# Performance work log

Hardware: AMD Instinct MI355X
Metric: run time of the kernel (lower is better)

The kernel has to match this reference:

```python
import jax, jax.numpy as jnp
import numpy as np
from jax import lax

CLAMP = 4.135
OUT = 7            # RoI pool output size
SCALE = 1.0 / 16.0 # feature-map stride 16


def bilinear_gather(feat, bidx, y, x):
    """feat [B,C,H,W]; bidx [N] int; y,x [N,Ph,Pw] coords in feature space -> [N,C,Ph,Pw]."""
    B, C, H, W = feat.shape
    y = jnp.clip(y, 0.0, H - 1.0)
    x = jnp.clip(x, 0.0, W - 1.0)
    y0 = jnp.floor(y); x0 = jnp.floor(x)
    y0i = y0.astype(jnp.int32); x0i = x0.astype(jnp.int32)
    y1i = jnp.minimum(y0i + 1, H - 1); x1i = jnp.minimum(x0i + 1, W - 1)
    wy1 = y - y0; wx1 = x - x0
    wy0 = 1.0 - wy1; wx0 = 1.0 - wx1
    flat = feat.transpose(0, 2, 3, 1).reshape(B * H * W, C)
    base = (bidx * (H * W))[:, None, None]
    def g(yy, xx):
        return flat[base + yy * W + xx]  # [N,Ph,Pw,C]
    out = ((wy0 * wx0)[..., None] * g(y0i, x0i)
           + (wy0 * wx1)[..., None] * g(y0i, x1i)
           + (wy1 * wx0)[..., None] * g(y1i, x0i)
           + (wy1 * wx1)[..., None] * g(y1i, x1i))
    return out.transpose(0, 3, 1, 2)


def roi_align(feat, boxes, bidx):
    """RoIAlign, sampling_ratio=1 (one bilinear sample per bin center)."""
    N = boxes.shape[0]
    b = boxes * SCALE
    x1, y1, x2, y2 = b[:, 0], b[:, 1], b[:, 2], b[:, 3]
    bw = jnp.maximum(x2 - x1, 1.0) / OUT
    bh = jnp.maximum(y2 - y1, 1.0) / OUT
    c = jnp.arange(OUT, dtype=feat.dtype) + 0.5
    ys = y1[:, None] + c * bh[:, None]   # [N,OUT]
    xs = x1[:, None] + c * bw[:, None]
    yg = jnp.broadcast_to(ys[:, :, None], (N, OUT, OUT))
    xg = jnp.broadcast_to(xs[:, None, :], (N, OUT, OUT))
    return bilinear_gather(feat, bidx, yg, xg)


def xyxy_to_rbox(b):
    cx = (b[:, 0] + b[:, 2]) * 0.5
    cy = (b[:, 1] + b[:, 3]) * 0.5
    w = b[:, 2] - b[:, 0]
    h = b[:, 3] - b[:, 1]
    return jnp.stack([cx, cy, w, h, jnp.zeros_like(cx)], axis=1)


def decode_deltas_to_rboxes(rboxes, deltas):
    cx, cy, w, h, a = (rboxes[:, i] for i in range(5))
    dx, dy, dw, dh, da = (deltas[:, i] for i in range(5))
    return jnp.stack([cx + dx * w, cy + dy * h,
                      w * jnp.exp(dw), h * jnp.exp(dh), a + da], axis=1)


def grid_sample_zeros(feat, gx, gy):
    """F.grid_sample(bilinear, padding_mode='zeros', align_corners=False).
    feat [N,C,H,W]; gx,gy [N,Ho,Wo] normalized coords -> [N,C,Ho,Wo]."""
    N, C, H, W = feat.shape
    ix = ((gx + 1.0) * W - 1.0) * 0.5
    iy = ((gy + 1.0) * H - 1.0) * 0.5
    x0 = jnp.floor(ix); y0 = jnp.floor(iy)
    wx1 = ix - x0; wy1 = iy - y0
    x0i = x0.astype(jnp.int32); y0i = y0.astype(jnp.int32)
    flat = feat.transpose(0, 2, 3, 1).reshape(N, H * W, C)
    Ho, Wo = gx.shape[1], gx.shape[2]
    def g(yy, xx, wt):
        valid = ((yy >= 0) & (yy < H) & (xx >= 0) & (xx < W)).astype(feat.dtype)
        idx = jnp.clip(yy, 0, H - 1) * W + jnp.clip(xx, 0, W - 1)
        v = jnp.take_along_axis(flat, idx.reshape(N, -1, 1), axis=1)
        v = v.reshape(N, Ho, Wo, C)
        return (wt * valid)[..., None] * v
    out = (g(y0i, x0i, (1 - wy1) * (1 - wx1))
           + g(y0i, x0i + 1, (1 - wy1) * wx1)
           + g(y0i + 1, x0i, wy1 * (1 - wx1))
           + g(y0i + 1, x0i + 1, wy1 * wx1))
    return out.transpose(0, 3, 1, 2)


def setup_inputs() -> dict:
    key = jax.random.key(0)
    ks = jax.random.split(key, 12)
    B, C, H, W = 2, 256, 64, 64
    N, NC = 2048, 16
    FD = C * OUT * OUT  # 12544
    features = jax.random.normal(ks[0], (B, C, H, W), jnp.float32)
    # valid image-space boxes (image 1024x1024, stride-16 features)
    cx = jax.random.uniform(ks[1], (N,), minval=96.0, maxval=928.0)
    cy = jax.random.uniform(ks[2], (N,), minval=96.0, maxval=928.0)
    bw = jax.random.uniform(ks[3], (N,), minval=16.0, maxval=128.0)
    bh = jax.random.uniform(ks[4], (N,), minval=16.0, maxval=128.0)
    proposals = jnp.stack([cx - bw / 2, cy - bh / 2, cx + bw / 2, cy + bh / 2], axis=1)
    batch_idx = jnp.repeat(jnp.arange(B, dtype=jnp.int32), N // B)
    s = 0.02
    return {
        "features": features,
        "proposals": proposals,
        "batch_idx": batch_idx,
        "conv_w": jax.random.normal(ks[5], (C, C, 3, 3), jnp.float32) * s,
        "conv_b": jnp.zeros((C,), jnp.float32),
        "align_w": jax.random.normal(ks[6], (5, FD), jnp.float32) * s,
        "align_b": jnp.zeros((5,), jnp.float32),
        "fc1_w": jax.random.normal(ks[7], (1024, FD), jnp.float32) * s,
        "fc1_b": jnp.zeros((1024,), jnp.float32),
        "fc2_w": jax.random.normal(ks[8], (1024, 1024), jnp.float32) * s,
        "fc2_b": jnp.zeros((1024,), jnp.float32),
        "cls_w": jax.random.normal(ks[9], (NC, 1024), jnp.float32) * s,
        "cls_b": jnp.zeros((NC,), jnp.float32),
        "box_w": jax.random.normal(ks[10], (5, 1024), jnp.float32) * s,
        "box_b": jnp.zeros((5,), jnp.float32),
    }


def reference(features, proposals, batch_idx, conv_w, conv_b, align_w, align_b,
              fc1_w, fc1_b, fc2_w, fc2_b, cls_w, cls_b, box_w, box_b):
    N = proposals.shape[0]
    # 1) RoI align
    box_feat = roi_align(features, proposals, batch_idx)           # [N,256,7,7]
    a = lax.conv_general_dilated(box_feat, conv_w, (1, 1), ((1, 1), (1, 1)),
                                 dimension_numbers=("NCHW", "OIHW", "NCHW"))
    a = jax.nn.relu(a + conv_b[None, :, None, None]).reshape(N, -1)
    coarse = jnp.clip(a @ align_w.T + align_b, -CLAMP, CLAMP)      # [N,5]
    # 3) decode to rboxes (torch.no_grad -> stop_gradient)
    prop_rb = xyxy_to_rbox(proposals)
    align_rb = lax.stop_gradient(decode_deltas_to_rboxes(prop_rb, coarse))
    # 4) affine grid from rbox (no translation, matches source) + grid_sample
    w, h, ang = align_rb[:, 2], align_rb[:, 3], align_rb[:, 4]
    cth, sth = jnp.cos(ang), jnp.sin(ang)
    sx, sy = w / OUT, h / OUT
    base = (2.0 * jnp.arange(OUT, dtype=box_feat.dtype) + 1.0) / OUT - 1.0
    xb = base[None, None, :]
    yb = base[None, :, None]
    gx = (sx * cth)[:, None, None] * xb + (-(sy * sth))[:, None, None] * yb
    gy = (sx * sth)[:, None, None] * xb + (sy * cth)[:, None, None] * yb
    aligned = grid_sample_zeros(box_feat, gx, gy)                  # [N,256,7,7]
    # 5) refine head MLP + predictors
    r = jax.nn.relu(aligned.reshape(N, -1) @ fc1_w.T + fc1_b)
    r = jax.nn.relu(r @ fc2_w.T + fc2_b)
    logits = r @ cls_w.T + cls_b                                   # [N,16]
    final = jnp.clip(r @ box_w.T + box_b, -CLAMP, CLAMP)           # [N,5]
    # 6) eval-path decode + softmax (per-class NMS is dynamic-shape postproc, excluded)
    pred_rboxes = decode_deltas_to_rboxes(prop_rb, final)
    scores = jax.nn.softmax(logits, axis=-1)
    return jnp.concatenate([pred_rboxes, scores], axis=1)          # [N,21]
```

## Files before the change

kernel.cpp:

```cpp
#include <hip/hip_runtime.h>
#include <hip/hip_bf16.h>
#include <math.h>
#include <type_traits>

constexpr int B = 2, C = 256, H = 64, W = 64, HW = H * W;
constexpr int N = 2048, OUT = 7, P = 49, FD = C * P;
constexpr int K1 = 1024;
constexpr float CLAMP_V = 4.135f, SCALE_V = 1.0f / 16.0f;
constexpr int LDB = 264;

typedef short s8v __attribute__((ext_vector_type(8)));
typedef short s4v __attribute__((ext_vector_type(4)));
typedef float f32x4 __attribute__((ext_vector_type(4)));

template <int I, int NN, class F>
__device__ __forceinline__ void static_for(F&& f) {
    if constexpr (I < NN) {
        f(std::integral_constant<int, I>{});
        static_for<I + 1, NN>(static_cast<F&&>(f));
    }
}

__device__ __forceinline__ int xcd_swz(int blk, int nblk) {
    const int cpx = nblk >> 3;
    return (blk & 7) * cpx + (blk >> 3);
}

__global__ void k_prep_all(const float* __restrict__ features, float* __restrict__ featT,
                           const float* __restrict__ conv_w, __hip_bfloat16* __restrict__ wB,
                           const float* __restrict__ align_w, float4* __restrict__ aw4,
                           float* __restrict__ aw1,
                           const float* __restrict__ fc1_w, __hip_bfloat16* __restrict__ fc1B,
                           const float* __restrict__ fc2_w, __hip_bfloat16* __restrict__ fc2B) {
    __shared__ float smem[64 * 49];
    const int id = blockIdx.x;
    const int t = threadIdx.x;
    if (id < 2048) {
        const int x = id % 128, y = (id / 128) % 8, b = id / 1024;
        const int c0 = y * 32, p0 = x * 32;
        const int tx = t % 32, ty = t / 32;
        float* tile = smem;
#pragma unroll
        for (int r = 0; r < 32; r += 8)
            tile[(ty + r) * 33 + tx] = features[(size_t)(b * C + c0 + ty + r) * HW + p0 + tx];
        __syncthreads();
#pragma unroll
        for (int r = 0; r < 32; r += 8)
            featT[(size_t)(b * HW + p0 + ty + r) * C + c0 + tx] = tile[tx * 33 + ty + r];
    } else if (id < 2120) {
        const int T = id - 2048;
        const int tap = T / 8, s = T % 8;
        const int co = t;
#pragma unroll
        for (int q = 0; q < 4; ++q)
#pragma unroll
            for (int j = 0; j < 8; ++j) {
                const int ci = s * 32 + q * 8 + j;
                wB[(((size_t)T * 256 + co) * 4 + q) * 8 + j] =
                    __float2bfloat16(conv_w[(size_t)co * 2304 + ci * 9 + tap]);
            }
    } else if (id < 2169) {
        const int o = id - 2120;
        const int co = t;
        float4 v;
        v.x = align_w[(size_t)0 * FD + co * 49 + o];
        v.y = align_w[(size_t)1 * FD + co * 49 + o];
        v.z = align_w[(size_t)2 * FD + co * 49 + o];
        v.w = align_w[(size_t)3 * FD + co * 49 + o];
        aw4[o * 256 + co] = v;
        aw1[o * 256 + co] = align_w[(size_t)4 * FD + co * 49 + o];
    } else if (id < 6265) {
        const int q = id - 2169;
        const int c0 = (q % 4) * 64;
        const int o = q / 4;
        const float* src = fc1_w + (size_t)o * FD + (size_t)c0 * 49;
        for (int i = t; i < 64 * 49; i += 256) smem[i] = src[i];
        __syncthreads();
        __hip_bfloat16* dst = fc1B + (size_t)o * FD + c0;
        for (int j = t; j < 64 * 49; j += 256) {
            const int p = j >> 6, cc = j & 63;
            dst[(size_t)p * 256 + cc] = __float2bfloat16(smem[cc * 49 + p]);
        }
    } else {
        const int bid = id - 6265;
        const int n4 = (K1 * K1) / 4;
        for (int i = bid * 256 + t; i < n4; i += 256 * 256) {
            const float4 v = reinterpret_cast<const float4*>(fc2_w)[i];
            fc2B[i * 4 + 0] = __float2bfloat16(v.x);
            fc2B[i * 4 + 1] = __float2bfloat16(v.y);
            fc2B[i * 4 + 2] = __float2bfloat16(v.z);
            fc2B[i * 4 + 3] = __float2bfloat16(v.w);
        }
    }
}

__global__ __launch_bounds__(256, 2) void k_roi_conv_grid(
    const float* __restrict__ featT, const float* __restrict__ proposals,
    const int* __restrict__ bidx, const __hip_bfloat16* __restrict__ wB,
    const float* __restrict__ conv_b, const float4* __restrict__ aw4,
    const float* __restrict__ aw1, const float* __restrict__ align_b,
    __hip_bfloat16* __restrict__ alignedOut) {
    __shared__ __align__(16) __hip_bfloat16 bfh[100 * LDB];
    __shared__ float red[64];

    const int blk = xcd_swz(blockIdx.x, 1024);
    const int t = threadIdx.x;
    const int lane = t & 63, wid = t >> 6;
    const int l15 = lane & 15;
    const int qofs = (lane >> 4) * 8;

#pragma unroll
    for (int r = 0; r < 2; ++r) {
        const int n = blk * 2 + r;
        const float px1 = proposals[n * 4 + 0] * SCALE_V, py1 = proposals[n * 4 + 1] * SCALE_V;
        const float px2 = proposals[n * 4 + 2] * SCALE_V, py2 = proposals[n * 4 + 3] * SCALE_V;
        const float bw = fmaxf(px2 - px1, 1.0f) * (1.0f / OUT);
        const float bh = fmaxf(py2 - py1, 1.0f) * (1.0f / OUT);
        const int b = bidx[n];
        const float* fb = featT + (size_t)b * HW * C;
#pragma unroll 2
        for (int p = wid; p < P; p += 4) {
            const int pyi = p / 7, pxi = p % 7;
            float y = py1 + (pyi + 0.5f) * bh;
            float x = px1 + (pxi + 0.5f) * bw;
            y = fminf(fmaxf(y, 0.f), (float)(H - 1));
            x = fminf(fmaxf(x, 0.f), (float)(W - 1));
            const float y0f = floorf(y), x0f = floorf(x);
            const int y0 = (int)y0f, x0 = (int)x0f;
            const int y1 = min(y0 + 1, H - 1), x1 = min(x0 + 1, W - 1);
            const float wy1 = y - y0f, wx1 = x - x0f;
            const float wy0 = 1.f - wy1, wx0 = 1.f - wx1;
            const int c4 = lane * 4;
            const float4 v00 = *reinterpret_cast<const float4*>(&fb[(size_t)(y0 * W + x0) * C + c4]);
            const float4 v01 = *reinterpret_cast<const float4*>(&fb[(size_t)(y0 * W + x1) * C + c4]);
            const float4 v10 = *reinterpret_cast<const float4*>(&fb[(size_t)(y1 * W + x0) * C + c4]);
            const float4 v11 = *reinterpret_cast<const float4*>(&fb[(size_t)(y1 * W + x1) * C + c4]);
            s4v o4;
            o4[0] = (short)__bfloat16_as_ushort(__float2bfloat16(
                        wy0 * (wx0 * v00.x + wx1 * v01.x) + wy1 * (wx0 * v10.x + wx1 * v11.x)));
            o4[1] = (short)__bfloat16_as_ushort(__float2bfloat16(
                        wy0 * (wx0 * v00.y + wx1 * v01.y) + wy1 * (wx0 * v10.y + wx1 * v11.y)));
            o4[2] = (short)__bfloat16_as_ushort(__float2bfloat16(
                        wy0 * (wx0 * v00.z + wx1 * v01.z) + wy1 * (wx0 * v10.z + wx1 * v11.z)));
            o4[3] = (short)__bfloat16_as_ushort(__float2bfloat16(
                        wy0 * (wx0 * v00.w + wx1 * v01.w) + wy1 * (wx0 * v10.w + wx1 * v11.w)));
            *reinterpret_cast<s4v*>(&bfh[(2 * p + r) * LDB + c4]) = o4;
        }
    }
    bfh[98 * LDB + t] = __float2bfloat16(0.f);
    bfh[99 * LDB + t] = __float2bfloat16(0.f);
    __syncthreads();

    const int rp = l15 & 1;
    int oyt[7], oxt[7];
    bool pval[7];
    static_for<0, 7>([&](auto MT) {
        const int p = (MT.value * 16 + l15) >> 1;
        pval[MT.value] = (p < 49);
        oyt[MT.value] = p / 7;
        oxt[MT.value] = p % 7;
    });
    int bofs[4];
    static_for<0, 4>([&](auto NT) {
        const int col = wid * 64 + NT.value * 16 + l15;
        bofs[NT.value] = col * 32 + qofs;
    });

    f32x4 acc[7][4] = {};
    for (int tap = 0; tap < 9; ++tap) {
        const int dy = tap / 3 - 1, dx = tap % 3 - 1;
        int rsel[7];
        static_for<0, 7>([&](auto MT) {
            const int iy = oyt[MT.value] + dy, ix = oxt[MT.value] + dx;
            const bool v = pval[MT.value] && ((unsigned)iy < 7u) && ((unsigned)ix < 7u);
            rsel[MT.value] = (v ? (2 * (iy * 7 + ix) + rp) : (98 + rp)) * LDB;
        });
        const __hip_bfloat16* wTap = wB + (size_t)tap * 8 * 8192;
#pragma unroll
        for (int s = 0; s < 8; ++s) {
            s8v af[7], bfr[4];
            static_for<0, 4>([&](auto NT) {
                bfr[NT.value] = *reinterpret_cast<const s8v*>(&wTap[(size_t)s * 8192 + bofs[NT.value]]);
            });
            static_for<0, 7>([&](auto MT) {
                af[MT.value] = *reinterpret_cast<const s8v*>(&bfh[rsel[MT.value] + s * 32 + qofs]);
            });
            __builtin_amdgcn_s_setprio(1);
            static_for<0, 7>([&](auto MT) {
                static_for<0, 4>([&](auto NT) {
                    acc[MT.value][NT.value] = __builtin_amdgcn_mfma_f32_16x16x32_bf16(
                        af[MT.value], bfr[NT.value], acc[MT.value][NT.value], 0, 0, 0);
                });
            });
            __builtin_amdgcn_s_setprio(0);
        }
    }

    const int hi = lane >> 4;
    float cb[4];
    static_for<0, 4>([&](auto NT) { cb[NT.value] = conv_b[wid * 64 + NT.value * 16 + l15]; });
    float pc[2][5] = {};
    static_for<0, 7>([&](auto MT) {
        static_for<0, 4>([&](auto RR) {
            constexpr int r = RR.value & 1;
            const int p = MT.value * 8 + hi * 2 + (RR.value >> 1);
            if (p < 49) {
                static_for<0, 4>([&](auto NT) {
                    const int co = wid * 64 + NT.value * 16 + l15;
                    const float4 w4 = aw4[p * 256 + co];
                    const float  w1 = aw1[p * 256 + co];
                    const float a = fmaxf(acc[MT.value][NT.value][RR.value] + cb[NT.value], 0.f);
                    pc[r][0] = fmaf(a, w4.x, pc[r][0]);
                    pc[r][1] = fmaf(a, w4.y, pc[r][1]);
                    pc[r][2] = fmaf(a, w4.z, pc[r][2]);
                    pc[r][3] = fmaf(a, w4.w, pc[r][3]);
                    pc[r][4] = fmaf(a, w1,   pc[r][4]);
                });
            }
        });
    });
    static_for<0, 2>([&](auto RI) {
        static_for<0, 5>([&](auto J) {
            float s = pc[RI.value][J.value];
#pragma unroll
            for (int off = 32; off; off >>= 1) s += __shfl_xor(s, off);
            pc[RI.value][J.value] = s;
        });
        if (lane == 0) {
            static_for<0, 5>([&](auto J) { red[RI.value * 20 + wid * 5 + J.value] = pc[RI.value][J.value]; });
        }
    });
    __syncthreads();

    if (t < 2) {
        const int r = t;
        const int n = blk * 2 + r;
        float coarse[5];
        static_for<0, 5>([&](auto Jc) {
            constexpr int j = Jc.value;
            float s = red[r * 20 + j] + red[r * 20 + 5 + j] + red[r * 20 + 10 + j] +
                      red[r * 20 + 15 + j] + align_b[j];
            coarse[j] = fminf(fmaxf(s, -CLAMP_V), CLAMP_V);
        });
        const float x1r = proposals[n * 4 + 0], y1r = proposals[n * 4 + 1];
        const float x2r = proposals[n * 4 + 2], y2r = proposals[n * 4 + 3];
        const float w = x2r - x1r, h = y2r - y1r;
        const float w2 = w * expf(coarse[2]);
        const float h2 = h * expf(coarse[3]);
        const float ang = coarse[4];
        const float cth = cosf(ang), sth = sinf(ang);
        const float sx = w2 * (1.0f / OUT), sy = h2 * (1.0f / OUT);
        red[48 + r * 4 + 0] = sx * cth;
        red[48 + r * 4 + 1] = sy * sth;
        red[48 + r * 4 + 2] = sx * sth;
        red[48 + r * 4 + 3] = sy * cth;
    }
    __syncthreads();

#pragma unroll
    for (int r = 0; r < 2; ++r) {
        const float gA = red[48 + r * 4 + 0], gBv = red[48 + r * 4 + 1];
        const float gC = red[48 + r * 4 + 2], gD = red[48 + r * 4 + 3];
        __hip_bfloat16* ao = alignedOut + (size_t)(blk * 2 + r) * FD;
        const int c4 = lane * 4;
#pragma unroll 2
        for (int p = wid; p < P; p += 4) {
            const int pyi = p / 7, pxi = p % 7;
            const float xb = (2 * pxi + 1) * (1.0f / OUT) - 1.0f;
            const float yb = (2 * pyi + 1) * (1.0f / OUT) - 1.0f;
            const float gx = gA * xb - gBv * yb;
            const float gy = gC * xb + gD * yb;
            const float ix = ((gx + 1.0f) * OUT - 1.0f) * 0.5f;
            const float iy = ((gy + 1.0f) * OUT - 1.0f) * 0.5f;
            const float x0f = floorf(ix), y0f = floorf(iy);
            const int x0 = (int)x0f, y0 = (int)y0f;
            const float wx1 = ix - x0f, wy1 = iy - y0f;
            const float wx0 = 1.f - wx1, wy0 = 1.f - wy1;
            const float w00 = wy0 * wx0, w01 = wy0 * wx1, w10 = wy1 * wx0, w11 = wy1 * wx1;
            const bool vx0 = (unsigned)x0 < 7u, vx1 = (unsigned)(x0 + 1) < 7u;
            const bool vy0 = (unsigned)y0 < 7u, vy1 = (unsigned)(y0 + 1) < 7u;
            const int r00 = (vy0 && vx0) ? (y0 * 7 + x0) : 49;
            const int r01 = (vy0 && vx1) ? (y0 * 7 + x0 + 1) : 49;
            const int r10 = (vy1 && vx0) ? ((y0 + 1) * 7 + x0) : 49;
            const int r11 = (vy1 && vx1) ? ((y0 + 1) * 7 + x0 + 1) : 49;
            const s4v b00 = *reinterpret_cast<const s4v*>(&bfh[(2 * r00 + r) * LDB + c4]);
            const s4v b01 = *reinterpret_cast<const s4v*>(&bfh[(2 * r01 + r) * LDB + c4]);
            const s4v b10 = *reinterpret_cast<const s4v*>(&bfh[(2 * r10 + r) * LDB + c4]);
            const s4v b11 = *reinterpret_cast<const s4v*>(&bfh[(2 * r11 + r) * LDB + c4]);
            s4v o4;
            static_for<0, 4>([&](auto J) {
                constexpr int j = J.value;
                float v = w00 * __bfloat162float(__ushort_as_bfloat16((unsigned short)b00[j]))
                        + w01 * __bfloat162float(__ushort_as_bfloat16((unsigned short)b01[j]))
                        + w10 * __bfloat162float(__ushort_as_bfloat16((unsigned short)b10[j]))
                        + w11 * __bfloat162float(__ushort_as_bfloat16((unsigned short)b11[j]));
                o4[j] = (short)__bfloat16_as_ushort(__float2bfloat16(v));
            });
            *reinterpret_cast<s4v*>(&ao[p * 256 + c4]) = o4;
        }
    }
}

template <int BM, int BN, int BK>
__global__ __launch_bounds__(256, 4) void k_gemm_bf16(
    const __hip_bfloat16* __restrict__ A, const __hip_bfloat16* __restrict__ Wt,
    const float* __restrict__ bias, float* __restrict__ CoutF,
    __hip_bfloat16* __restrict__ CoutH, int M, int Nn, int K, int relu) {
    constexpr int LD = BK + 8;
    __shared__ __align__(16) __hip_bfloat16 As[2][BM * LD];
    __shared__ __align__(16) __hip_bfloat16 Ws[2][BN * LD];
    const int ntb = Nn / BN;
    const int blkS = xcd_swz(blockIdx.x, gridDim.x);
    const int bx = blkS % ntb, by = blkS / ntb;
    const int t = threadIdx.x;
    const int lane = t & 63, wid = t >> 6;
    const int l15 = lane & 15;
    const int qofs = (lane >> 4) * 8;
    const int wm = wid >> 1, wn = wid & 1;

    const int ar = t >> 3, ak = (t & 7) * 8;
    const size_t aBase = (size_t)(by * BM) * K;
    const size_t bBase = (size_t)(bx * BN) * K;

    f32x4 acc[2][2] = {};

    const int steps = K / BK;
    {
        const s8v a0 = *reinterpret_cast<const s8v*>(&A[aBase + (size_t)ar * K + ak]);
        const s8v a1 = *reinterpret_cast<const s8v*>(&A[aBase + (size_t)(ar + 32) * K + ak]);
        const s8v b0 = *reinterpret_cast<const s8v*>(&Wt[bBase + (size_t)ar * K + ak]);
        const s8v b1 = *reinterpret_cast<const s8v*>(&Wt[bBase + (size_t)(ar + 32) * K + ak]);
        *reinterpret_cast<s8v*>(&As[0][ar * LD + ak]) = a0;
        *reinterpret_cast<s8v*>(&As[0][(ar + 32) * LD + ak]) = a1;
        *reinterpret_cast<s8v*>(&Ws[0][ar * LD + ak]) = b0;
        *reinterpret_cast<s8v*>(&Ws[0][(ar + 32) * LD + ak]) = b1;
    }
    __syncthreads();

    for (int s = 0; s < steps; ++s) {
        const int cur = s & 1;
        const bool pf = (s + 1 < steps);
        s8v a0, a1, b0, b1;
        if (pf) {
            const int k0 = (s + 1) * BK;
            a0 = *reinterpret_cast<const s8v*>(&A[aBase + (size_t)ar * K + k0 + ak]);
            a1 = *reinterpret_cast<const s8v*>(&A[aBase + (size_t)(ar + 32) * K + k0 + ak]);
            b0 = *reinterpret_cast<const s8v*>(&Wt[bBase + (size_t)ar * K + k0 + ak]);
            b1 = *reinterpret_cast<const s8v*>(&Wt[bBase + (size_t)(ar + 32) * K + k0 + ak]);
        }
        static_for<0, 2>([&](auto KH) {
            s8v afr[2], bfr[2];
            static_for<0, 2>([&](auto MT) {
                afr[MT.value] = *reinterpret_cast<const s8v*>(
                    &As[cur][(wm * 32 + MT.value * 16 + l15) * LD + KH.value * 32 + qofs]);
            });
            static_for<0, 2>([&](auto NT) {
                bfr[NT.value] = *reinterpret_cast<const s8v*>(
                    &Ws[cur][(wn * 32 + NT.value * 16 + l15) * LD + KH.value * 32 + qofs]);
            });
            static_for<0, 2>([&](auto MT) {
                static_for<0, 2>([&](auto NT) {
                    acc[MT.value][NT.value] = __builtin_amdgcn_mfma_f32_16x16x32_bf16(
                        afr[MT.value], bfr[NT.value], acc[MT.value][NT.value], 0, 0, 0);
                });
            });
        });
        if (pf) {
            __syncthreads();
            const int nxt = cur ^ 1;
            *reinterpret_cast<s8v*>(&As[nxt][ar * LD + ak]) = a0;
            *reinterpret_cast<s8v*>(&As[nxt][(ar + 32) * LD + ak]) = a1;
            *reinterpret_cast<s8v*>(&Ws[nxt][ar * LD + ak]) = b0;
            *reinterpret_cast<s8v*>(&Ws[nxt][(ar + 32) * LD + ak]) = b1;
            __syncthreads();
        }
    }

    static_for<0, 2>([&](auto MT) {
        static_for<0, 2>([&](auto NT) {
            const int col = bx * BN + wn * 32 + NT.value * 16 + l15;
            const float bv = bias[col];
            static_for<0, 4>([&](auto RR) {
                const int row = by * BM + wm * 32 + MT.value * 16 + (lane >> 4) * 4 + RR.value;
                float v = acc[MT.value][NT.value][RR.value] + bv;
                if (relu) v = fmaxf(v, 0.f);
                if (CoutF) CoutF[(size_t)row * Nn + col] = v;
                if (CoutH) CoutH[(size_t)row * Nn + col] = __float2bfloat16(v);
            });
        });
    });
}

__global__ void k_heads(const float* __restrict__ r2, const float* __restrict__ cls_w,
                        const float* __restrict__ cls_b, const float* __restrict__ box_w,
                        const float* __restrict__ box_b, const float* __restrict__ proposals,
                        float* __restrict__ out) {
    const int n = blockIdx.x;
    const int t = threadIdx.x;
    const float* r = r2 + (size_t)n * K1;
    float rv[16];
    static_for<0, 16>([&](auto Jc) { rv[Jc.value] = r[t + 64 * Jc.value]; });
    float s[21];
    static_for<0, 21>([&](auto Oc) {
        constexpr int o = Oc.value;
        const float* w = (o < 16) ? (cls_w + (size_t)o * K1) : (box_w + (size_t)(o - 16) * K1);
        float a = 0.f;
        static_for<0, 16>([&](auto Jc) { a = fmaf(rv[Jc.value], w[t + 64 * Jc.value], a); });
#pragma unroll
        for (int off = 32; off; off >>= 1) a += __shfl_xor(a, off);
        s[o] = a;
    });
    float logits[16];
    float m = -1e30f;
    static_for<0, 16>([&](auto Oc) {
        logits[Oc.value] = s[Oc.value] + cls_b[Oc.value];
        m = fmaxf(m, logits[Oc.value]);
    });
    float es = 0.f;
    static_for<0, 16>([&](auto Oc) {
        logits[Oc.value] = expf(logits[Oc.value] - m);
        es += logits[Oc.value];
    });
    const float inv = 1.0f / es;
    float fdelta[5];
    static_for<0, 5>([&](auto Jc) {
        fdelta[Jc.value] = fminf(fmaxf(s[16 + Jc.value] + box_b[Jc.value], -CLAMP_V), CLAMP_V);
    });
    const float x1r = proposals[n * 4 + 0], y1r = proposals[n * 4 + 1];
    const float x2r = proposals[n * 4 + 2], y2r = proposals[n * 4 + 3];
    const float cx = (x1r + x2r) * 0.5f, cy = (y1r + y2r) * 0.5f;
    const float w = x2r - x1r, h = y2r - y1r;
    float pred[5];
    pred[0] = cx + fdelta[0] * w;
    pred[1] = cy + fdelta[1] * h;
    pred[2] = w * expf(fdelta[2]);
    pred[3] = h * expf(fdelta[3]);
    pred[4] = fdelta[4];
    float* orow = out + (size_t)n * 21;
    static_for<0, 5>([&](auto Oc) {
        if (t == Oc.value) orow[Oc.value] = pred[Oc.value];
    });
    static_for<0, 16>([&](auto Oc) {
        if (t == 5 + Oc.value) orow[5 + Oc.value] = logits[Oc.value] * inv;
    });
}

extern "C" void kernel_launch(void* const* d_in, const int* in_sizes, int n_in,
                              void* d_out, int out_size, void* d_ws, size_t ws_size,
                              hipStream_t stream) {
    (void)in_sizes; (void)n_in; (void)out_size; (void)ws_size;
    const float* features  = (const float*)d_in[0];
    const float* proposals = (const float*)d_in[1];
    const int*   batch_idx = (const int*)d_in[2];
    const float* conv_w    = (const float*)d_in[3];
    const float* conv_b    = (const float*)d_in[4];
    const float* align_w   = (const float*)d_in[5];
    const float* align_b   = (const float*)d_in[6];
    const float* fc1_w     = (const float*)d_in[7];
    const float* fc1_b     = (const float*)d_in[8];
    const float* fc2_w     = (const float*)d_in[9];
    const float* fc2_b     = (const float*)d_in[10];
    const float* cls_w     = (const float*)d_in[11];
    const float* cls_b     = (const float*)d_in[12];
    const float* box_w     = (const float*)d_in[13];
    const float* box_b     = (const float*)d_in[14];
    float* out = (float*)d_out;

    float* ws    = (float*)d_ws;
    float* featT = ws;
    float* r2    = featT + (size_t)B * HW * C;
    float4* aw4  = (float4*)(r2 + (size_t)N * K1);
    float* aw1   = (float*)(aw4 + 49 * 256);
    __hip_bfloat16* alignedH = (__hip_bfloat16*)(aw1 + 49 * 256);
    __hip_bfloat16* r1H   = alignedH + (size_t)N * FD;
    __hip_bfloat16* wB    = r1H + (size_t)N * K1;
    __hip_bfloat16* fc1B  = wB + 2304 * 256;
    __hip_bfloat16* fc2B  = fc1B + (size_t)K1 * FD;

    k_prep_all<<<6521, 256, 0, stream>>>(features, featT, conv_w, wB, align_w, aw4, aw1,
                                         fc1_w, fc1B, fc2_w, fc2B);
    k_roi_conv_grid<<<N / 2, 256, 0, stream>>>(featT, proposals, batch_idx, wB, conv_b,
                                               aw4, aw1, align_b, alignedH);
    k_gemm_bf16<64, 64, 64><<<(N / 64) * (K1 / 64), 256, 0, stream>>>(
        alignedH, fc1B, fc1_b, nullptr, r1H, N, K1, FD, 1);
    k_gemm_bf16<64, 64, 64><<<(N / 64) * (K1 / 64), 256, 0, stream>>>(
        r1H, fc2B, fc2_b, r2, nullptr, N, K1, K1, 1);
    k_heads<<<N, 64, 0, stream>>>(r2, cls_w, cls_b, box_w, box_b, proposals, out);
}
```

Baseline: 301.6 us.

## Pre-swizzle FC weights into MFMA fragment layout and read B directly from global

The prep kernel now writes fc1 and fc2 weights in bf16, laid out so each lane's 8-element MFMA B fragment is one contiguous 16-byte vector. The GEMM kernel drops the shared-memory staging of the weight tile and loads B fragments straight from global memory, which halves LDS use and removes the weight stores to LDS. The tradeoff is that global B loads now sit in the inner loop without prefetch, so they may expose latency. The fc1 prep also changes to one block per output row, staging the whole row in LDS.

```diff
diff --git a/kernel.cpp b/kernel.cpp
--- a/kernel.cpp
+++ b/kernel.cpp
@@ -30,9 +30,9 @@
                            const float* __restrict__ conv_w, __hip_bfloat16* __restrict__ wB,
                            const float* __restrict__ align_w, float4* __restrict__ aw4,
                            float* __restrict__ aw1,
-                           const float* __restrict__ fc1_w, __hip_bfloat16* __restrict__ fc1B,
-                           const float* __restrict__ fc2_w, __hip_bfloat16* __restrict__ fc2B) {
-    __shared__ float smem[64 * 49];
+                           const float* __restrict__ fc1_w, __hip_bfloat16* __restrict__ fc1Bf,
+                           const float* __restrict__ fc2_w, __hip_bfloat16* __restrict__ fc2Bf) {
+    __shared__ float smem[6272];
     const int id = blockIdx.x;
     const int t = threadIdx.x;
     if (id < 2048) {
@@ -69,27 +69,36 @@
         v.w = align_w[(size_t)3 * FD + co * 49 + o];
         aw4[o * 256 + co] = v;
         aw1[o * 256 + co] = align_w[(size_t)4 * FD + co * 49 + o];
-    } else if (id < 6265) {
-        const int q = id - 2169;
-        const int c0 = (q % 4) * 64;
-        const int o = q / 4;
-        const float* src = fc1_w + (size_t)o * FD + (size_t)c0 * 49;
-        for (int i = t; i < 64 * 49; i += 256) smem[i] = src[i];
+    } else if (id < 3193) {
+        const int o = id - 2169;
+        __hip_bfloat16* rowh = (__hip_bfloat16*)smem;
+        const float* src = fc1_w + (size_t)o * FD;
+        for (int i = t; i < FD; i += 256) rowh[i] = __float2bfloat16(src[i]);
         __syncthreads();
-        __hip_bfloat16* dst = fc1B + (size_t)o * FD + c0;
-        for (int j = t; j < 64 * 49; j += 256) {
-            const int p = j >> 6, cc = j & 63;
-            dst[(size_t)p * 256 + cc] = __float2bfloat16(smem[cc * 49 + p]);
+        const int ct = o >> 4, c16 = o & 15;
+        for (int i = t; i < FD / 8; i += 256) {
+            const int k0 = i * 8;
+            const int kb = k0 >> 5, qq = (k0 >> 3) & 3;
+            s8v v;
+            static_for<0, 8>([&](auto J) {
+                const int k = k0 + J.value;
+                const int cf = k & 255, p = k >> 8;
+                v[J.value] = (short)__bfloat16_as_ushort(rowh[cf * 49 + p]);
+            });
+            *reinterpret_cast<s8v*>(fc1Bf + ((((size_t)kb * 64 + ct) * 4 + qq) * 16 + c16) * 8) = v;
         }
     } else {
-        const int bid = id - 6265;
-        const int n4 = (K1 * K1) / 4;
-        for (int i = bid * 256 + t; i < n4; i += 256 * 256) {
-            const float4 v = reinterpret_cast<const float4*>(fc2_w)[i];
-            fc2B[i * 4 + 0] = __float2bfloat16(v.x);
-            fc2B[i * 4 + 1] = __float2bfloat16(v.y);
-            fc2B[i * 4 + 2] = __float2bfloat16(v.z);
-            fc2B[i * 4 + 3] = __float2bfloat16(v.w);
+        const int o = id - 3193;
+        const float* src = fc2_w + (size_t)o * K1;
+        const int ct = o >> 4, c16 = o & 15;
+        for (int i = t; i < K1 / 8; i += 256) {
+            const int k0 = i * 8;
+            const int kb = k0 >> 5, qq = (k0 >> 3) & 3;
+            s8v v;
+            static_for<0, 8>([&](auto J) {
+                v[J.value] = (short)__bfloat16_as_ushort(__float2bfloat16(src[k0 + J.value]));
+            });
+            *reinterpret_cast<s8v*>(fc2Bf + ((((size_t)kb * 64 + ct) * 4 + qq) * 16 + c16) * 8) = v;
         }
     }
 }
@@ -303,24 +312,27 @@
 
 template <int BM, int BN, int BK>
 __global__ __launch_bounds__(256, 4) void k_gemm_bf16(
-    const __hip_bfloat16* __restrict__ A, const __hip_bfloat16* __restrict__ Wt,
+    const __hip_bfloat16* __restrict__ A, const __hip_bfloat16* __restrict__ Bf,
     const float* __restrict__ bias, float* __restrict__ CoutF,
     __hip_bfloat16* __restrict__ CoutH, int M, int Nn, int K, int relu) {
     constexpr int LD = BK + 8;
     __shared__ __align__(16) __hip_bfloat16 As[2][BM * LD];
-    __shared__ __align__(16) __hip_bfloat16 Ws[2][BN * LD];
     const int ntb = Nn / BN;
     const int blkS = xcd_swz(blockIdx.x, gridDim.x);
     const int bx = blkS % ntb, by = blkS / ntb;
     const int t = threadIdx.x;
     const int lane = t & 63, wid = t >> 6;
     const int l15 = lane & 15;
-    const int qofs = (lane >> 4) * 8;
+    const int qq = lane >> 4;
+    const int qofs = qq * 8;
     const int wm = wid >> 1, wn = wid & 1;
 
     const int ar = t >> 3, ak = (t & 7) * 8;
     const size_t aBase = (size_t)(by * BM) * K;
-    const size_t bBase = (size_t)(bx * BN) * K;
+    const int nct = Nn >> 4;
+    const s8v* Bv = reinterpret_cast<const s8v*>(Bf);
+    int ctab[2];
+    static_for<0, 2>([&](auto NT) { ctab[NT.value] = bx * (BN / 16) + wn * 2 + NT.value; });
 
     f32x4 acc[2][2] = {};
 
@@ -328,35 +340,29 @@
     {
         const s8v a0 = *reinterpret_cast<const s8v*>(&A[aBase + (size_t)ar * K + ak]);
         const s8v a1 = *reinterpret_cast<const s8v*>(&A[aBase + (size_t)(ar + 32) * K + ak]);
-        const s8v b0 = *reinterpret_cast<const s8v*>(&Wt[bBase + (size_t)ar * K + ak]);
-        const s8v b1 = *reinterpret_cast<const s8v*>(&Wt[bBase + (size_t)(ar + 32) * K + ak]);
         *reinterpret_cast<s8v*>(&As[0][ar * LD + ak]) = a0;
         *reinterpret_cast<s8v*>(&As[0][(ar + 32) * LD + ak]) = a1;
-        *reinterpret_cast<s8v*>(&Ws[0][ar * LD + ak]) = b0;
-        *reinterpret_cast<s8v*>(&Ws[0][(ar + 32) * LD + ak]) = b1;
     }
     __syncthreads();
 
     for (int s = 0; s < steps; ++s) {
         const int cur = s & 1;
         const bool pf = (s + 1 < steps);
-        s8v a0, a1, b0, b1;
+        s8v a0, a1;
         if (pf) {
             const int k0 = (s + 1) * BK;
             a0 = *reinterpret_cast<const s8v*>(&A[aBase + (size_t)ar * K + k0 + ak]);
             a1 = *reinterpret_cast<const s8v*>(&A[aBase + (size_t)(ar + 32) * K + k0 + ak]);
-            b0 = *reinterpret_cast<const s8v*>(&Wt[bBase + (size_t)ar * K + k0 + ak]);
-            b1 = *reinterpret_cast<const s8v*>(&Wt[bBase + (size_t)(ar + 32) * K + k0 + ak]);
         }
         static_for<0, 2>([&](auto KH) {
+            const int kb = s * 2 + KH.value;
             s8v afr[2], bfr[2];
             static_for<0, 2>([&](auto MT) {
                 afr[MT.value] = *reinterpret_cast<const s8v*>(
                     &As[cur][(wm * 32 + MT.value * 16 + l15) * LD + KH.value * 32 + qofs]);
             });
             static_for<0, 2>([&](auto NT) {
-                bfr[NT.value] = *reinterpret_cast<const s8v*>(
-                    &Ws[cur][(wn * 32 + NT.value * 16 + l15) * LD + KH.value * 32 + qofs]);
+                bfr[NT.value] = Bv[((size_t)kb * nct + ctab[NT.value]) * 64 + qq * 16 + l15];
             });
             static_for<0, 2>([&](auto MT) {
                 static_for<0, 2>([&](auto NT) {
@@ -370,8 +376,6 @@
             const int nxt = cur ^ 1;
             *reinterpret_cast<s8v*>(&As[nxt][ar * LD + ak]) = a0;
             *reinterpret_cast<s8v*>(&As[nxt][(ar + 32) * LD + ak]) = a1;
-            *reinterpret_cast<s8v*>(&Ws[nxt][ar * LD + ak]) = b0;
-            *reinterpret_cast<s8v*>(&Ws[nxt][(ar + 32) * LD + ak]) = b1;
             __syncthreads();
         }
     }
@@ -474,16 +478,16 @@
     __hip_bfloat16* alignedH = (__hip_bfloat16*)(aw1 + 49 * 256);
     __hip_bfloat16* r1H   = alignedH + (size_t)N * FD;
     __hip_bfloat16* wB    = r1H + (size_t)N * K1;
-    __hip_bfloat16* fc1B  = wB + 2304 * 256;
-    __hip_bfloat16* fc2B  = fc1B + (size_t)K1 * FD;
-
-    k_prep_all<<<6521, 256, 0, stream>>>(features, featT, conv_w, wB, align_w, aw4, aw1,
-                                         fc1_w, fc1B, fc2_w, fc2B);
+    __hip_bfloat16* fc1Bf = wB + 2304 * 256;
+    __hip_bfloat16* fc2Bf = fc1Bf + (size_t)K1 * FD;
+
+    k_prep_all<<<4217, 256, 0, stream>>>(features, featT, conv_w, wB, align_w, aw4, aw1,
+                                         fc1_w, fc1Bf, fc2_w, fc2Bf);
     k_roi_conv_grid<<<N / 2, 256, 0, stream>>>(featT, proposals, batch_idx, wB, conv_b,
                                                aw4, aw1, align_b, alignedH);
     k_gemm_bf16<64, 64, 64><<<(N / 64) * (K1 / 64), 256, 0, stream>>>(
-        alignedH, fc1B, fc1_b, nullptr, r1H, N, K1, FD, 1);
+        alignedH, fc1Bf, fc1_b, nullptr, r1H, N, K1, FD, 1);
     k_gemm_bf16<64, 64, 64><<<(N / 64) * (K1 / 64), 256, 0, stream>>>(
-        r1H, fc2B, fc2_b, r2, nullptr, N, K1, K1, 1);
+        r1H, fc2Bf, fc2_b, r2, nullptr, N, K1, K1, 1);
     k_heads<<<N, 64, 0, stream>>>(r2, cls_w, cls_b, box_w, box_b, proposals, out);
 }
```

New measurement: 381.0 us. 26.3% more time.
